# Optimization experiments

Hardware: AMD Instinct MI355X
Metric: run time of the kernel (lower is better)

## Reference

```python
import jax, jax.numpy as jnp
import numpy as np


def _sru(x, W, bf, br):
    # x: (B, T, D); W: (D, 3H) with D == H (highway needs matching dims)
    B, T, D = x.shape
    H = bf.shape[0]
    U = jnp.einsum('btd,dk->btk', x, W)  # (B, T, 3H)
    x_tilde, f_pre, r_pre = jnp.split(U, 3, axis=-1)
    f = jax.nn.sigmoid(f_pre + bf)  # forget gate
    r = jax.nn.sigmoid(r_pre + br)  # reset (highway) gate

    def step(c, inp):
        f_t, xt_t = inp
        c = f_t * c + (1.0 - f_t) * xt_t
        return c, c

    c0 = jnp.zeros((B, H), x.dtype)
    # scan over time (time-major)
    _, cs = jax.lax.scan(step, c0, (jnp.swapaxes(f, 0, 1), jnp.swapaxes(x_tilde, 0, 1)))
    c = jnp.swapaxes(cs, 0, 1)  # (B, T, H)
    h = r * c + (1.0 - r) * x  # highway connection
    return h


def setup_inputs() -> dict:
    key = jax.random.key(0)
    ks = jax.random.split(key, 3)
    B, T, D = 32, 2000, 512
    Dg, Hg = D // 2, D // 2
    scale = 1.0 / np.sqrt(Dg)
    x = jax.random.normal(ks[0], (B, T, D), dtype=jnp.float32)
    W1 = jax.random.normal(ks[1], (Dg, 3 * Hg), dtype=jnp.float32) * scale
    W2 = jax.random.normal(ks[2], (Dg, 3 * Hg), dtype=jnp.float32) * scale
    bf1 = jnp.zeros((Hg,), jnp.float32)
    br1 = jnp.zeros((Hg,), jnp.float32)
    bf2 = jnp.zeros((Hg,), jnp.float32)
    br2 = jnp.zeros((Hg,), jnp.float32)
    return {"x": x, "W1": W1, "bf1": bf1, "br1": br1, "W2": W2, "bf2": bf2, "br2": br2}


def reference(x, W1, bf1, br1, W2, bf2, br2):
    # GRNN: split channels in half, run an SRU on each half, concat outputs
    x1, x2 = jnp.split(x, 2, axis=-1)
    y1 = _sru(x1, W1, bf1, br1)
    y2 = _sru(x2, W2, bf2, br2)
    return jnp.concatenate([y1, y2], axis=-1)
```

## Files before the change

### kernel.cpp

```cpp
#include <hip/hip_runtime.h>
#include <hip/hip_bf16.h>
#include <math.h>


constexpr int TLEN  = 2000;
constexpr int DDIM  = 512;
constexpr int HH    = 256;
constexpr int N3    = 768;
constexpr int MROWS = 64000;

typedef __attribute__((ext_vector_type(8))) short bf16x8;
typedef __attribute__((ext_vector_type(4))) float f32x4;

__device__ __forceinline__ short f2bf(float f) {
    __hip_bfloat16 h = __float2bfloat16(f);
    return *reinterpret_cast<short*>(&h);
}
__device__ __forceinline__ float sigmoidf_(float v) {
    return 1.0f / (1.0f + __expf(-v));
}

__global__ __launch_bounds__(256) void gemm_gates(
    const float* __restrict__ x,
    const float* __restrict__ W1, const float* __restrict__ bf1, const float* __restrict__ br1,
    const float* __restrict__ W2, const float* __restrict__ bf2, const float* __restrict__ br2,
    __hip_bfloat16* __restrict__ xt_ws, __hip_bfloat16* __restrict__ f_ws,
    float* __restrict__ out)
{
    const int half = blockIdx.z;
    const float* __restrict__ W   = half ? W2  : W1;
    const float* __restrict__ bfb = half ? bf2 : bf1;
    const float* __restrict__ brb = half ? br2 : br1;

    const int id  = blockIdx.x;
    const int swz = (id & 7) * 375 + (id >> 3);
    const int n0  = (swz % 6) * 128;
    const int m0  = (swz / 6) * 128;

    __shared__ short Als[128 * 40];
    __shared__ short Bls[128 * 40];

    const int tid = threadIdx.x;
    const int l   = tid & 63;
    const int w   = tid >> 6;
    const int wm  = w >> 1, wn = w & 1;
    const int lr  = l & 15;
    const int lk  = (l >> 4) * 8;

    f32x4 acc[4][4];
#pragma unroll
    for (int mi = 0; mi < 4; ++mi)
#pragma unroll
        for (int ni = 0; ni < 4; ++ni) acc[mi][ni] = (f32x4){0.f, 0.f, 0.f, 0.f};

    const int arow = tid >> 1;
    const int akh  = (tid & 1) * 16;
    const float* aptr = x + (size_t)(m0 + arow) * DDIM + half * HH + akh;
    const int bk   = tid >> 3;
    const int bng0 = tid & 7;

    for (int k0 = 0; k0 < HH; k0 += 32) {
        {
            const float4 v0 = *reinterpret_cast<const float4*>(aptr + k0 + 0);
            const float4 v1 = *reinterpret_cast<const float4*>(aptr + k0 + 4);
            const float4 v2 = *reinterpret_cast<const float4*>(aptr + k0 + 8);
            const float4 v3 = *reinterpret_cast<const float4*>(aptr + k0 + 12);
            bf16x8 p0, p1;
            p0[0]=f2bf(v0.x); p0[1]=f2bf(v0.y); p0[2]=f2bf(v0.z); p0[3]=f2bf(v0.w);
            p0[4]=f2bf(v1.x); p0[5]=f2bf(v1.y); p0[6]=f2bf(v1.z); p0[7]=f2bf(v1.w);
            p1[0]=f2bf(v2.x); p1[1]=f2bf(v2.y); p1[2]=f2bf(v2.z); p1[3]=f2bf(v2.w);
            p1[4]=f2bf(v3.x); p1[5]=f2bf(v3.y); p1[6]=f2bf(v3.z); p1[7]=f2bf(v3.w);
            short* dst = &Als[arow * 40 + akh];
            *reinterpret_cast<bf16x8*>(dst)     = p0;
            *reinterpret_cast<bf16x8*>(dst + 8) = p1;
        }
#pragma unroll
        for (int i = 0; i < 4; ++i) {
            const int ng = bng0 + 8 * i;
            const float4 v = *reinterpret_cast<const float4*>(
                W + (size_t)(k0 + bk) * N3 + n0 + ng * 4);
            Bls[(ng * 4 + 0) * 40 + bk] = f2bf(v.x);
            Bls[(ng * 4 + 1) * 40 + bk] = f2bf(v.y);
            Bls[(ng * 4 + 2) * 40 + bk] = f2bf(v.z);
            Bls[(ng * 4 + 3) * 40 + bk] = f2bf(v.w);
        }
        __syncthreads();

        bf16x8 af[4], bfr[4];
#pragma unroll
        for (int mi = 0; mi < 4; ++mi)
            af[mi] = *reinterpret_cast<const bf16x8*>(
                &Als[(wm * 64 + mi * 16 + lr) * 40 + lk]);
#pragma unroll
        for (int ni = 0; ni < 4; ++ni)
            bfr[ni] = *reinterpret_cast<const bf16x8*>(
                &Bls[(wn * 64 + ni * 16 + lr) * 40 + lk]);
#pragma unroll
        for (int mi = 0; mi < 4; ++mi)
#pragma unroll
            for (int ni = 0; ni < 4; ++ni)
                acc[mi][ni] = __builtin_amdgcn_mfma_f32_16x16x32_bf16(
                    af[mi], bfr[ni], acc[mi][ni], 0, 0, 0);
        __syncthreads();
    }

    const int seg = n0 >> 8;
#pragma unroll
    for (int mi = 0; mi < 4; ++mi) {
        const int rowb = m0 + wm * 64 + mi * 16 + (l >> 4) * 4;
#pragma unroll
        for (int ni = 0; ni < 4; ++ni) {
            const int col  = wn * 64 + ni * 16 + lr;
            const int hcol = (n0 & 255) + col;
            const f32x4 a = acc[mi][ni];
            if (seg == 0) {
#pragma unroll
                for (int q = 0; q < 4; ++q) {
                    const size_t idx = (size_t)(rowb + q) * DDIM + half * HH + hcol;
                    xt_ws[idx] = __float2bfloat16(a[q]);
                }
            } else if (seg == 1) {
                const float bias = bfb[hcol];
#pragma unroll
                for (int q = 0; q < 4; ++q) {
                    const size_t idx = (size_t)(rowb + q) * DDIM + half * HH + hcol;
                    f_ws[idx] = __float2bfloat16(sigmoidf_(a[q] + bias));
                }
            } else {
                const float bias = brb[hcol];
#pragma unroll
                for (int q = 0; q < 4; ++q) {
                    const size_t idx = (size_t)(rowb + q) * DDIM + half * HH + hcol;
                    out[idx] = sigmoidf_(a[q] + bias);
                }
            }
        }
    }
}

__global__ __launch_bounds__(1024) void scan_highway(
    const float* __restrict__ x,
    const __hip_bfloat16* __restrict__ xt_ws, const __hip_bfloat16* __restrict__ f_ws,
    float* __restrict__ out)
{
    __shared__ float smP[16][64];
    __shared__ float smS[16][64];

    const int tid = threadIdx.x;
    const int sl  = tid & 63;
    const int ch  = tid >> 6;
    const int s   = blockIdx.x * 64 + sl;
    const int b   = s >> 9;
    const int col = s & 511;
    const size_t base = (size_t)b * TLEN * DDIM + col;
    const size_t idx0 = base + (size_t)(ch * 125) * DDIM;

    float P = 1.f, S = 0.f;
    if (ch < 15) {
        size_t idx = idx0;
#pragma unroll 5
        for (int t = 0; t < 125; ++t, idx += DDIM) {
            const float f  = __bfloat162float(f_ws[idx]);
            const float xt = __bfloat162float(xt_ws[idx]);
            S = __builtin_fmaf(f, S, __builtin_fmaf(-f, xt, xt));
            P *= f;
        }
    }
    smP[ch][sl] = P;
    smS[ch][sl] = S;
    __syncthreads();

    float c = 0.f;
    for (int j = 0; j < ch; ++j)
        c = __builtin_fmaf(smP[j][sl], c, smS[j][sl]);

    size_t idx = idx0;
#pragma unroll 5
    for (int t = 0; t < 125; ++t, idx += DDIM) {
        const float f  = __bfloat162float(f_ws[idx]);
        const float xt = __bfloat162float(xt_ws[idx]);
        c = __builtin_fmaf(f, c, __builtin_fmaf(-f, xt, xt));
        const float r  = out[idx];
        const float xv = x[idx];
        out[idx] = __builtin_fmaf(r, c - xv, xv);
    }
}

extern "C" void kernel_launch(void* const* d_in, const int* in_sizes, int n_in,
                              void* d_out, int out_size, void* d_ws, size_t ws_size,
                              hipStream_t stream)
{
    const float* x   = (const float*)d_in[0];
    const float* W1  = (const float*)d_in[1];
    const float* bf1 = (const float*)d_in[2];
    const float* br1 = (const float*)d_in[3];
    const float* W2  = (const float*)d_in[4];
    const float* bf2 = (const float*)d_in[5];
    const float* br2 = (const float*)d_in[6];
    float* out = (float*)d_out;

    const size_t elems = (size_t)MROWS * DDIM;
    __hip_bfloat16* xt_ws = (__hip_bfloat16*)d_ws;
    __hip_bfloat16* f_ws  = xt_ws + elems;

    gemm_gates<<<dim3(3000, 1, 2), 256, 0, stream>>>(
        x, W1, bf1, br1, W2, bf2, br2, xt_ws, f_ws, out);
    scan_highway<<<256, 1024, 0, stream>>>(x, xt_ws, f_ws, out);
}
```

Baseline: 496.3 us.

## Fuse gate GEMM with scan prep, pre-transpose weights, split scan into passes

Adds a weight pre-transpose/bf16 conversion kernel. The GEMM is restructured so each block computes the x_tilde, f and r columns for the same 64 hidden units over a 125-row time chunk. The epilogue packs f and (1-f)*x_tilde into a single 32-bit bf16 pair. The scan becomes three kernels with many more blocks (chunk summaries, a carry combine, and a vectorized apply pass), replacing the 256-block single-kernel scan. This cuts intermediate traffic and raises scan parallelism, at the cost of extra launches and padded GEMM rows (125 of 128 used); the old path remains as a fallback when the workspace is too small.

```diff
diff --git a/kernel.cpp b/kernel.cpp
--- a/kernel.cpp
+++ b/kernel.cpp
@@ -1,6 +1,7 @@
 #include <hip/hip_runtime.h>
 #include <hip/hip_bf16.h>
 #include <math.h>
+#include <stdint.h>
 
 
 constexpr int TLEN  = 2000;
@@ -8,6 +9,13 @@
 constexpr int HH    = 256;
 constexpr int N3    = 768;
 constexpr int MROWS = 64000;
+constexpr int CHUNK = 125;
+
+constexpr size_t FU_OFF = 0;
+constexpr size_t WT_OFF = 131072000;
+constexpr size_t PS_OFF = WT_OFF + 786432;
+constexpr size_t C0_OFF = PS_OFF + 2097152;
+constexpr size_t WS_NEED = C0_OFF + 1048576;
 
 typedef __attribute__((ext_vector_type(8))) short bf16x8;
 typedef __attribute__((ext_vector_type(4))) float f32x4;
@@ -20,25 +28,37 @@
     return 1.0f / (1.0f + __expf(-v));
 }
 
-__global__ __launch_bounds__(256) void gemm_gates(
-    const float* __restrict__ x,
-    const float* __restrict__ W1, const float* __restrict__ bf1, const float* __restrict__ br1,
-    const float* __restrict__ W2, const float* __restrict__ bf2, const float* __restrict__ br2,
-    __hip_bfloat16* __restrict__ xt_ws, __hip_bfloat16* __restrict__ f_ws,
-    float* __restrict__ out)
-{
-    const int half = blockIdx.z;
-    const float* __restrict__ W   = half ? W2  : W1;
+__global__ __launch_bounds__(256) void prep_w(
+    const float* __restrict__ W1, const float* __restrict__ W2,
+    __hip_bfloat16* __restrict__ Wt)
+{
+    const int gid  = blockIdx.x * 256 + threadIdx.x;
+    const int j8   = gid & 31;
+    const int col  = (gid >> 5) % N3;
+    const int half = gid / (32 * N3);
+    const float* __restrict__ W = half ? W2 : W1;
+
+    bf16x8 v;
+#pragma unroll
+    for (int jj = 0; jj < 8; ++jj)
+        v[jj] = f2bf(W[(size_t)(j8 * 8 + jj) * N3 + col]);
+    *reinterpret_cast<bf16x8*>(Wt + ((size_t)half * N3 + col) * 256 + j8 * 8) = v;
+}
+
+__global__ __launch_bounds__(256) void gemm_scanprep(
+    const float* __restrict__ x, const __hip_bfloat16* __restrict__ Wt,
+    const float* __restrict__ bf1, const float* __restrict__ br1,
+    const float* __restrict__ bf2, const float* __restrict__ br2,
+    uint32_t* __restrict__ fu, float* __restrict__ out)
+{
+    const int nt      = blockIdx.x;
+    const int chunkid = blockIdx.y;
+    const int half    = blockIdx.z;
     const float* __restrict__ bfb = half ? bf2 : bf1;
     const float* __restrict__ brb = half ? br2 : br1;
 
-    const int id  = blockIdx.x;
-    const int swz = (id & 7) * 375 + (id >> 3);
-    const int n0  = (swz % 6) * 128;
-    const int m0  = (swz / 6) * 128;
-
-    __shared__ short Als[128 * 40];
-    __shared__ short Bls[128 * 40];
+    __shared__ short Als[128 * 72];
+    __shared__ short Bls[192 * 64];
 
     const int tid = threadIdx.x;
     const int l   = tid & 63;
@@ -47,18 +67,197 @@
     const int lr  = l & 15;
     const int lk  = (l >> 4) * 8;
 
+    f32x4 acc[3][4][2];
+#pragma unroll
+    for (int s = 0; s < 3; ++s)
+#pragma unroll
+        for (int mi = 0; mi < 4; ++mi)
+#pragma unroll
+            for (int ni = 0; ni < 2; ++ni) acc[s][mi][ni] = (f32x4){0.f,0.f,0.f,0.f};
+
+    const int arowL = tid >> 4;
+    const int kq    = tid & 15;
+
+    for (int ks = 0; ks < 4; ++ks) {
+#pragma unroll
+        for (int ps = 0; ps < 8; ++ps) {
+            const int rl = ps * 16 + arowL;
+            int g = chunkid * CHUNK + rl;
+            if (g > MROWS - 1) g = MROWS - 1;
+            const float4 v = *reinterpret_cast<const float4*>(
+                x + (size_t)g * DDIM + half * HH + ks * 64 + kq * 4);
+            short4 p;
+            p.x = f2bf(v.x); p.y = f2bf(v.y); p.z = f2bf(v.z); p.w = f2bf(v.w);
+            *reinterpret_cast<short4*>(&Als[rl * 72 + kq * 4]) = p;
+        }
+#pragma unroll
+        for (int i = 0; i < 6; ++i) {
+            const int gidx = tid + i * 256;
+            const int row  = gidx >> 3;
+            const int j8   = gidx & 7;
+            const int seg  = row >> 6;
+            const int n    = row & 63;
+            const bf16x8 v = *reinterpret_cast<const bf16x8*>(
+                Wt + ((size_t)half * N3 + seg * 256 + nt * 64 + n) * 256 + ks * 64 + j8 * 8);
+            const int dst = row * 64 + ((j8 * 8) ^ ((n & 7) << 3));
+            *reinterpret_cast<bf16x8*>(&Bls[dst]) = v;
+        }
+        __syncthreads();
+
+#pragma unroll
+        for (int kk = 0; kk < 2; ++kk) {
+            bf16x8 af[4];
+#pragma unroll
+            for (int mi = 0; mi < 4; ++mi)
+                af[mi] = *reinterpret_cast<const bf16x8*>(
+                    &Als[(wm * 64 + mi * 16 + lr) * 72 + kk * 32 + lk]);
+#pragma unroll
+            for (int seg = 0; seg < 3; ++seg)
+#pragma unroll
+                for (int ni = 0; ni < 2; ++ni) {
+                    const int n = wn * 32 + ni * 16 + lr;
+                    const bf16x8 bv = *reinterpret_cast<const bf16x8*>(
+                        &Bls[(seg * 64 + n) * 64 + ((kk * 32 + lk) ^ ((n & 7) << 3))]);
+#pragma unroll
+                    for (int mi = 0; mi < 4; ++mi)
+                        acc[seg][mi][ni] = __builtin_amdgcn_mfma_f32_16x16x32_bf16(
+                            af[mi], bv, acc[seg][mi][ni], 0, 0, 0);
+                }
+        }
+        __syncthreads();
+    }
+
+#pragma unroll
+    for (int mi = 0; mi < 4; ++mi) {
+        const int rl0 = wm * 64 + mi * 16 + (l >> 4) * 4;
+#pragma unroll
+        for (int ni = 0; ni < 2; ++ni) {
+            const int col = nt * 64 + wn * 32 + ni * 16 + lr;
+            const float bfv = bfb[col];
+            const float brv = brb[col];
+            const f32x4 aX = acc[0][mi][ni];
+            const f32x4 aF = acc[1][mi][ni];
+            const f32x4 aR = acc[2][mi][ni];
+#pragma unroll
+            for (int q = 0; q < 4; ++q) {
+                const int rl = rl0 + q;
+                if (rl < CHUNK) {
+                    const size_t row = (size_t)chunkid * CHUNK + rl;
+                    const size_t idx = row * DDIM + half * HH + col;
+                    const float xt = aX[q];
+                    const float f  = sigmoidf_(aF[q] + bfv);
+                    const float r  = sigmoidf_(aR[q] + brv);
+                    const float u  = xt - f * xt;
+                    const uint32_t pk = ((uint32_t)(uint16_t)f2bf(u) << 16)
+                                      | (uint16_t)f2bf(f);
+                    fu[idx]  = pk;
+                    out[idx] = r;
+                }
+            }
+        }
+    }
+}
+
+__global__ __launch_bounds__(256) void scan_pass1(
+    const uint32_t* __restrict__ fu, float2* __restrict__ pstab)
+{
+    const int col = blockIdx.x * 64 + (threadIdx.x & 63);
+    const int ch  = blockIdx.y * 4 + (threadIdx.x >> 6);
+    if (ch >= 15) return;
+    const int b = col >> 9, c = col & 511;
+    size_t idx = ((size_t)b * TLEN + ch * CHUNK) * DDIM + c;
+
+    float P = 1.f, S = 0.f;
+#pragma unroll 5
+    for (int t = 0; t < CHUNK; ++t, idx += DDIM) {
+        const uint32_t wv = fu[idx];
+        const float f = __uint_as_float(wv << 16);
+        const float u = __uint_as_float(wv & 0xffff0000u);
+        S = __builtin_fmaf(f, S, u);
+        P *= f;
+    }
+    pstab[ch * 16384 + col] = make_float2(P, S);
+}
+
+__global__ __launch_bounds__(256) void scan_combine(
+    const float2* __restrict__ pstab, float* __restrict__ c0tab)
+{
+    const int col = blockIdx.x * 256 + threadIdx.x;
+    float c = 0.f;
+#pragma unroll
+    for (int ch = 0; ch < 16; ++ch) {
+        c0tab[ch * 16384 + col] = c;
+        if (ch < 15) {
+            const float2 ps = pstab[ch * 16384 + col];
+            c = __builtin_fmaf(ps.x, c, ps.y);
+        }
+    }
+}
+
+__global__ __launch_bounds__(256) void scan_pass2(
+    const float* __restrict__ x, const uint32_t* __restrict__ fu,
+    const float* __restrict__ c0tab, float* __restrict__ out)
+{
+    const int cp = blockIdx.x * 64 + (threadIdx.x & 63);
+    const int ch = blockIdx.y * 4 + (threadIdx.x >> 6);
+    const int b  = cp >> 8;
+    const int c  = (cp & 255) * 2;
+    const int gcol = b * DDIM + c;
+    size_t idx = ((size_t)b * TLEN + ch * CHUNK) * DDIM + c;
+
+    float c0 = c0tab[ch * 16384 + gcol];
+    float c1 = c0tab[ch * 16384 + gcol + 1];
+#pragma unroll 5
+    for (int t = 0; t < CHUNK; ++t, idx += DDIM) {
+        const uint2  wv = *reinterpret_cast<const uint2*>(fu + idx);
+        const float2 rv = *reinterpret_cast<const float2*>(out + idx);
+        const float2 xv = *reinterpret_cast<const float2*>(x + idx);
+        const float f0 = __uint_as_float(wv.x << 16);
+        const float u0 = __uint_as_float(wv.x & 0xffff0000u);
+        const float f1 = __uint_as_float(wv.y << 16);
+        const float u1 = __uint_as_float(wv.y & 0xffff0000u);
+        c0 = __builtin_fmaf(f0, c0, u0);
+        c1 = __builtin_fmaf(f1, c1, u1);
+        float2 h;
+        h.x = __builtin_fmaf(rv.x, c0 - xv.x, xv.x);
+        h.y = __builtin_fmaf(rv.y, c1 - xv.y, xv.y);
+        *reinterpret_cast<float2*>(out + idx) = h;
+    }
+}
+
+__global__ __launch_bounds__(256) void gemm_gates_v3(
+    const float* __restrict__ x,
+    const float* __restrict__ W1, const float* __restrict__ bf1, const float* __restrict__ br1,
+    const float* __restrict__ W2, const float* __restrict__ bf2, const float* __restrict__ br2,
+    __hip_bfloat16* __restrict__ xt_ws, __hip_bfloat16* __restrict__ f_ws,
+    float* __restrict__ out)
+{
+    const int half = blockIdx.z;
+    const float* __restrict__ W   = half ? W2  : W1;
+    const float* __restrict__ bfb = half ? bf2 : bf1;
+    const float* __restrict__ brb = half ? br2 : br1;
+    const int id  = blockIdx.x;
+    const int swz = (id & 7) * 375 + (id >> 3);
+    const int n0  = (swz % 6) * 128;
+    const int m0  = (swz / 6) * 128;
+    __shared__ short Als[128 * 40];
+    __shared__ short Bls[128 * 40];
+    const int tid = threadIdx.x;
+    const int l   = tid & 63;
+    const int w   = tid >> 6;
+    const int wm  = w >> 1, wn = w & 1;
+    const int lr  = l & 15;
+    const int lk  = (l >> 4) * 8;
     f32x4 acc[4][4];
 #pragma unroll
     for (int mi = 0; mi < 4; ++mi)
 #pragma unroll
         for (int ni = 0; ni < 4; ++ni) acc[mi][ni] = (f32x4){0.f, 0.f, 0.f, 0.f};
-
     const int arow = tid >> 1;
     const int akh  = (tid & 1) * 16;
     const float* aptr = x + (size_t)(m0 + arow) * DDIM + half * HH + akh;
     const int bk   = tid >> 3;
     const int bng0 = tid & 7;
-
     for (int k0 = 0; k0 < HH; k0 += 32) {
         {
             const float4 v0 = *reinterpret_cast<const float4*>(aptr + k0 + 0);
@@ -85,7 +284,6 @@
             Bls[(ng * 4 + 3) * 40 + bk] = f2bf(v.w);
         }
         __syncthreads();
-
         bf16x8 af[4], bfr[4];
 #pragma unroll
         for (int mi = 0; mi < 4; ++mi)
@@ -103,7 +301,6 @@
                     af[mi], bfr[ni], acc[mi][ni], 0, 0, 0);
         __syncthreads();
     }
-
     const int seg = n0 >> 8;
 #pragma unroll
     for (int mi = 0; mi < 4; ++mi) {
@@ -138,14 +335,13 @@
     }
 }
 
-__global__ __launch_bounds__(1024) void scan_highway(
+__global__ __launch_bounds__(1024) void scan_highway_v3(
     const float* __restrict__ x,
     const __hip_bfloat16* __restrict__ xt_ws, const __hip_bfloat16* __restrict__ f_ws,
     float* __restrict__ out)
 {
     __shared__ float smP[16][64];
     __shared__ float smS[16][64];
-
     const int tid = threadIdx.x;
     const int sl  = tid & 63;
     const int ch  = tid >> 6;
@@ -153,13 +349,12 @@
     const int b   = s >> 9;
     const int col = s & 511;
     const size_t base = (size_t)b * TLEN * DDIM + col;
-    const size_t idx0 = base + (size_t)(ch * 125) * DDIM;
-
+    const size_t idx0 = base + (size_t)(ch * CHUNK) * DDIM;
     float P = 1.f, S = 0.f;
     if (ch < 15) {
         size_t idx = idx0;
 #pragma unroll 5
-        for (int t = 0; t < 125; ++t, idx += DDIM) {
+        for (int t = 0; t < CHUNK; ++t, idx += DDIM) {
             const float f  = __bfloat162float(f_ws[idx]);
             const float xt = __bfloat162float(xt_ws[idx]);
             S = __builtin_fmaf(f, S, __builtin_fmaf(-f, xt, xt));
@@ -169,14 +364,12 @@
     smP[ch][sl] = P;
     smS[ch][sl] = S;
     __syncthreads();
-
     float c = 0.f;
     for (int j = 0; j < ch; ++j)
         c = __builtin_fmaf(smP[j][sl], c, smS[j][sl]);
-
     size_t idx = idx0;
 #pragma unroll 5
-    for (int t = 0; t < 125; ++t, idx += DDIM) {
+    for (int t = 0; t < CHUNK; ++t, idx += DDIM) {
         const float f  = __bfloat162float(f_ws[idx]);
         const float xt = __bfloat162float(xt_ws[idx]);
         c = __builtin_fmaf(f, c, __builtin_fmaf(-f, xt, xt));
@@ -198,12 +391,26 @@
     const float* bf2 = (const float*)d_in[5];
     const float* br2 = (const float*)d_in[6];
     float* out = (float*)d_out;
-
-    const size_t elems = (size_t)MROWS * DDIM;
-    __hip_bfloat16* xt_ws = (__hip_bfloat16*)d_ws;
-    __hip_bfloat16* f_ws  = xt_ws + elems;
-
-    gemm_gates<<<dim3(3000, 1, 2), 256, 0, stream>>>(
-        x, W1, bf1, br1, W2, bf2, br2, xt_ws, f_ws, out);
-    scan_highway<<<256, 1024, 0, stream>>>(x, xt_ws, f_ws, out);
-}
+    char* ws = (char*)d_ws;
+
+    if (ws_size >= WS_NEED) {
+        uint32_t*       fu    = (uint32_t*)(ws + FU_OFF);
+        __hip_bfloat16* Wt    = (__hip_bfloat16*)(ws + WT_OFF);
+        float2*         pstab = (float2*)(ws + PS_OFF);
+        float*          c0tab = (float*)(ws + C0_OFF);
+
+        prep_w<<<192, 256, 0, stream>>>(W1, W2, Wt);
+        gemm_scanprep<<<dim3(4, 512, 2), 256, 0, stream>>>(
+            x, Wt, bf1, br1, bf2, br2, fu, out);
+        scan_pass1<<<dim3(256, 4), 256, 0, stream>>>(fu, pstab);
+        scan_combine<<<64, 256, 0, stream>>>(pstab, c0tab);
+        scan_pass2<<<dim3(128, 4), 256, 0, stream>>>(x, fu, c0tab, out);
+    } else {
+        const size_t elems = (size_t)MROWS * DDIM;
+        __hip_bfloat16* xt_ws = (__hip_bfloat16*)d_ws;
+        __hip_bfloat16* f_ws  = xt_ws + elems;
+        gemm_gates_v3<<<dim3(3000, 1, 2), 256, 0, stream>>>(
+            x, W1, bf1, br1, W2, bf2, br2, xt_ws, f_ws, out);
+        scan_highway_v3<<<256, 1024, 0, stream>>>(x, xt_ws, f_ws, out);
+    }
+}
```

Result: no change. 499.8 us (+0.7%).
